# Kernel optimization log

Measured on AMD Instinct MI355X. Metric: run time of the kernel, lower is better.

Reference implementation:

```python
import math
import jax, jax.numpy as jnp
import numpy as np

B, S, HID = 1, 2048, 2048
NH, QLR, KVLR = 16, 1536, 512
QKD, QKP, VD = 128, 64, 128          # nope dim, rope dim, v dim
IH, ID, TOPK = 4, 128, 512            # indexer heads, indexer head dim, topk
EPS = 1e-6
NEG = -1e9
_MS = 0.1 * 1.0 * math.log(40.0) + 1.0           # mscale adjustment, rope_factor=40
SCALE = _MS * _MS / math.sqrt(QKD + QKP)          # main attention softmax scale
IDX_SCALE = ID ** -0.5                            # indexer softmax scale


def _freqs_cos_sin():
    # seqlen <= original_max_position_embeddings -> plain RoPE freqs (no YaRN branch)
    freqs = 1.0 / (10000.0 ** (jnp.arange(0, QKP, 2, dtype=jnp.float32) / QKP))  # [QKP/2]
    ang = jnp.outer(jnp.arange(S, dtype=jnp.float32), freqs)                      # [S, QKP/2]
    return jnp.cos(ang)[None, :, None, :], jnp.sin(ang)[None, :, None, :]         # [1,S,1,QKP/2]


def _rope_interleaved(x, cos, sin):
    # pairs are (x[..., 2i], x[..., 2i+1])
    x1, x2 = x[..., 0::2], x[..., 1::2]
    yr = x1 * cos - x2 * sin
    yi = x1 * sin + x2 * cos
    return jnp.stack([yr, yi], axis=-1).reshape(x.shape)


def _rope_half(x, cos, sin):
    # interleaved=False: real = first half, imag = second half; output [reals..., imags...]
    d2 = x.shape[-1] // 2
    x1, x2 = x[..., :d2], x[..., d2:]
    return jnp.concatenate([x1 * cos - x2 * sin, x1 * sin + x2 * cos], axis=-1)


def _rmsnorm(x, w):
    return x * jax.lax.rsqrt(jnp.mean(x * x, axis=-1, keepdims=True) + EPS) * w


def _layernorm(x, w, b):
    m = jnp.mean(x, axis=-1, keepdims=True)
    v = jnp.mean((x - m) ** 2, axis=-1, keepdims=True)
    return (x - m) * jax.lax.rsqrt(v + EPS) * w + b


def _indexer(x, qr, cos, sin, mask3, idx_wq_b, idx_wk, idx_kn_w, idx_kn_b, idx_ww):
    # x, qr detached by caller. mask3: [B,S,S]
    q = (qr @ idx_wq_b.T).reshape(B, S, IH, ID)
    q_pe, q_nope = q[..., :QKP], q[..., QKP:]
    q_pe = _rope_half(q_pe, cos, sin)
    q = jnp.concatenate([q_pe, q_nope], axis=-1)                   # [B,S,IH,ID]
    k = _layernorm(x @ idx_wk.T, idx_kn_w, idx_kn_b)               # [B,S,ID]
    k_pe, k_nope = k[..., :QKP], k[..., QKP:]
    k_pe = _rope_half(k_pe[:, :, None, :], cos, sin)[:, :, 0, :]
    k = jnp.concatenate([k_pe, k_nope], axis=-1)                   # [B,S,ID]
    weights = (x @ idx_ww.T) * (IH ** -0.5)                        # [B,S,IH]
    logits = jnp.einsum('bthd,bsd->bths', q, k) * IDX_SCALE        # [B,T,IH,S]
    logits = jax.nn.relu(logits)
    logits = jnp.einsum('bths,bth->bts', logits, weights)          # weighted head sum
    logits = logits + mask3
    topk_vals, topk_idx = jax.lax.top_k(logits, TOPK)
    log_topk_prob = jax.nn.log_softmax(topk_vals, axis=-1)
    return topk_idx, log_topk_prob


def reference(hidden_states, attention_mask, wq_down, q_ln_w, wq_up, wkv_down,
              kv_ln_w, wk_up, wv_up, wo, idx_wq_b, idx_wk, idx_kn_w, idx_kn_b, idx_ww):
    x = jnp.swapaxes(hidden_states, 0, 1)                          # [B,S,HID]
    mask3 = attention_mask[:, 0]                                   # [B,S,S]
    cos, sin = _freqs_cos_sin()

    qr = _rmsnorm(x @ wq_down.T, q_ln_w)                           # [B,S,QLR]
    q = (qr @ wq_up.T).reshape(B, S, NH, QKD + QKP)
    q_nope, q_pe = q[..., :QKD], q[..., QKD:]
    q_pe = _rope_interleaved(q_pe, cos, sin)

    kv = x @ wkv_down.T                                            # [B,S,KVLR+QKP]
    kv_c, k_pe = kv[..., :KVLR], kv[..., KVLR:]
    kv_c = _rmsnorm(kv_c, kv_ln_w)
    k_pe = _rope_interleaved(k_pe[:, :, None, :], cos, sin)        # [B,S,1,QKP]

    k_up_w = wk_up.reshape(NH, QKD, KVLR)
    q_abs = jnp.einsum('bshd,hdc->bshc', q_nope, k_up_w)           # absorbed q
    q_abs = jnp.concatenate([q_abs, q_pe], axis=-1)                # [B,S,NH,KVLR+QKP]

    topk_idx, log_topk_prob = _indexer(
        jax.lax.stop_gradient(x), jax.lax.stop_gradient(qr), cos, sin, mask3,
        idx_wq_b, idx_wk, idx_kn_w, idx_kn_b, idx_ww)

    keys = jnp.concatenate([kv_c, k_pe[:, :, 0, :]], axis=-1)      # [B,T,KVLR+QKP]
    scores = jnp.einsum('bshd,btd->bsht', q_abs, keys) * SCALE     # [B,S,NH,T]
    scores = scores + mask3[:, :, None, :]
    bi = jnp.arange(B)[:, None, None]
    si = jnp.arange(S)[None, :, None]
    index_mask = jnp.full((B, S, S), NEG, jnp.float32).at[bi, si, topk_idx].set(0.0)
    scores = scores + index_mask[:, :, None, :]
    probs = jax.nn.softmax(scores, axis=-1)                        # [B,S,NH,T]
    attn_out = jnp.einsum('bsht,btd->bshd', probs, kv_c)           # values = kv_c

    idx4 = jnp.broadcast_to(topk_idx[:, :, None, :], (B, S, NH, TOPK))
    sparse_probs = jnp.take_along_axis(jax.lax.stop_gradient(probs), idx4, axis=-1)
    attn_score = sparse_probs.sum(axis=2)
    attn_score = attn_score / attn_score.sum(axis=-1, keepdims=True)
    tgt = jnp.clip(jnp.log(attn_score), -100.0, 0.0)
    inp = jnp.clip(log_topk_prob, -100.0, 0.0)
    kl = jnp.sum(jnp.exp(tgt) * (tgt - inp))

    v_up_w = wv_up.reshape(NH, VD, KVLR)
    attn_out = jnp.einsum('bshc,hdc->bshd', attn_out, v_up_w)
    out = attn_out.reshape(B, S, NH * VD) @ wo.T
    return jnp.swapaxes(out, 0, 1), kl


def setup_inputs():
    key = jax.random.key(0)
    ks = jax.random.split(key, 12)
    p = lambda k, sh: jax.random.normal(k, sh, jnp.float32) * 0.02
    hidden_states = jax.random.normal(ks[0], (S, B, HID), jnp.float32)
    causal = jnp.where(jnp.arange(S)[:, None] >= jnp.arange(S)[None, :], 0.0, NEG).astype(jnp.float32)
    attention_mask = jnp.broadcast_to(causal, (B, 1, S, S))
    return dict(
        hidden_states=hidden_states,
        attention_mask=attention_mask,
        wq_down=p(ks[1], (QLR, HID)),
        q_ln_w=jnp.ones((QLR,), jnp.float32),
        wq_up=p(ks[2], (NH * (QKD + QKP), QLR)),
        wkv_down=p(ks[3], (KVLR + QKP, HID)),
        kv_ln_w=jnp.ones((KVLR,), jnp.float32),
        wk_up=p(ks[4], (NH * QKD, KVLR)),
        wv_up=p(ks[5], (NH * VD, KVLR)),
        wo=p(ks[6], (HID, NH * VD)),
        idx_wq_b=p(ks[7], (IH * ID, QLR)),
        idx_wk=p(ks[8], (ID, HID)),
        idx_kn_w=jnp.ones((ID,), jnp.float32),
        idx_kn_b=jnp.zeros((ID,), jnp.float32),
        idx_ww=p(ks[9], (IH, HID)),
    )
```

## Files before the change

kernel.cpp:

```cpp
#include <hip/hip_runtime.h>
#include <hip/hip_bf16.h>
#include <math.h>

typedef __hip_bfloat16 bf16;
typedef __attribute__((ext_vector_type(8))) short short8v;
typedef __attribute__((ext_vector_type(4))) float f32x4;

static constexpr float EPS_   = 1e-6f;
static constexpr float NEG_   = -1000000000.0f;
static constexpr float SCALE_ = 0.13523378f;
static constexpr float IDXSC_ = 0.08838834764832f;
static constexpr double LN10K_32 = 0.28782313662425575;

#define MFMA16(a, b, c) __builtin_amdgcn_mfma_f32_16x16x32_bf16(a, b, c, 0, 0, 0)

static __device__ float block_reduce_op(float v, int op) {
  __shared__ float red_s[16];
  int lane = threadIdx.x & 63, wid = threadIdx.x >> 6;
  #pragma unroll
  for (int off = 32; off > 0; off >>= 1) {
    float o = __shfl_down(v, off);
    v = op ? fmaxf(v, o) : (v + o);
  }
  __syncthreads();
  if (lane == 0) red_s[wid] = v;
  __syncthreads();
  if (threadIdx.x == 0) {
    int nw = ((int)blockDim.x + 63) >> 6;
    float r = red_s[0];
    for (int i = 1; i < nw; i++) r = op ? fmaxf(r, red_s[i]) : (r + red_s[i]);
    red_s[0] = r;
  }
  __syncthreads();
  return red_s[0];
}

__global__ __launch_bounds__(256) void f2b_kernel(const float* __restrict__ in,
                                                  bf16* __restrict__ out, long n) {
  long i = ((long)blockIdx.x * 256 + threadIdx.x) * 4;
  if (i + 3 < n) {
    float4 v = *(const float4*)(in + i);
    out[i] = __float2bfloat16(v.x); out[i+1] = __float2bfloat16(v.y);
    out[i+2] = __float2bfloat16(v.z); out[i+3] = __float2bfloat16(v.w);
  } else {
    for (int j = 0; j < 4 && i + j < n; j++) out[i+j] = __float2bfloat16(in[i+j]);
  }
}

template <int BT, int OB>
__global__ __launch_bounds__(256) void gemm_bf16(
    const bf16* __restrict__ A, const bf16* __restrict__ B, void* __restrict__ Cv,
    int M, int N, int K, int lda, int ldb, int ldc, long sA, long sB, long sC) {
  A += (long)blockIdx.z * sA;
  B += (long)blockIdx.z * sB;
  __shared__ bf16 As[128][40];
  __shared__ bf16 Bs[128][40];
  const int m0 = blockIdx.y * 128, n0 = blockIdx.x * 128;
  const int tid = threadIdx.x;
  const int wave = tid >> 6, lane = tid & 63, g = lane >> 4, li = lane & 15;
  const int mB = (wave >> 1) * 64, nB = (wave & 1) * 64;
  f32x4 acc[4][4];
  #pragma unroll
  for (int i = 0; i < 4; i++)
    #pragma unroll
    for (int j = 0; j < 4; j++) acc[i][j] = (f32x4){0.f, 0.f, 0.f, 0.f};

  for (int k0 = 0; k0 < K; k0 += 32) {
    {
      int row = tid >> 1, ko = (tid & 1) * 16;
      const bf16* src = A + (long)(m0 + row) * lda + k0 + ko;
      *(short8v*)&As[row][ko]     = *(const short8v*)src;
      *(short8v*)&As[row][ko + 8] = *(const short8v*)(src + 8);
    }
    if (BT) {
      int row = tid >> 1, ko = (tid & 1) * 16;
      int rr = n0 + row; if (rr >= N) rr = N - 1;
      const bf16* src = B + (long)rr * ldb + k0 + ko;
      *(short8v*)&Bs[row][ko]     = *(const short8v*)src;
      *(short8v*)&Bs[row][ko + 8] = *(const short8v*)(src + 8);
    } else {
      int k = tid >> 3, nb = (tid & 7) * 16;
      const bf16* src = B + (long)(k0 + k) * ldb + n0 + nb;
      short8v v0 = *(const short8v*)src;
      short8v v1 = *(const short8v*)(src + 8);
      #pragma unroll
      for (int j = 0; j < 8; j++) {
        Bs[nb + j][k]     = ((const bf16*)&v0)[j];
        Bs[nb + 8 + j][k] = ((const bf16*)&v1)[j];
      }
    }
    __syncthreads();
    short8v af[4], bfr[4];
    #pragma unroll
    for (int mt = 0; mt < 4; mt++) af[mt]  = *(const short8v*)&As[mB + mt*16 + li][g*8];
    #pragma unroll
    for (int nt = 0; nt < 4; nt++) bfr[nt] = *(const short8v*)&Bs[nB + nt*16 + li][g*8];
    #pragma unroll
    for (int mt = 0; mt < 4; mt++)
      #pragma unroll
      for (int nt = 0; nt < 4; nt++)
        acc[mt][nt] = MFMA16(af[mt], bfr[nt], acc[mt][nt]);
    __syncthreads();
  }
  #pragma unroll
  for (int mt = 0; mt < 4; mt++)
    #pragma unroll
    for (int nt = 0; nt < 4; nt++)
      #pragma unroll
      for (int r = 0; r < 4; r++) {
        int row = m0 + mB + mt*16 + g*4 + r;
        int col = n0 + nB + nt*16 + li;
        if (col < N) {
          long off = (long)blockIdx.z * sC + (long)row * ldc + col;
          if (OB) ((bf16*)Cv)[off] = __float2bfloat16(acc[mt][nt][r]);
          else    ((float*)Cv)[off] = acc[mt][nt][r];
        }
      }
}

__global__ __launch_bounds__(256) void rmsnorm_b_kernel(const float* __restrict__ x,
                                                        const float* __restrict__ w,
                                                        bf16* __restrict__ out, int D) {
  const float* r = x + (long)blockIdx.x * D;
  bf16* o = out + (long)blockIdx.x * D;
  float ss = 0.f;
  for (int i = threadIdx.x; i < D; i += 256) { float v = r[i]; ss = fmaf(v, v, ss); }
  ss = block_reduce_op(ss, 0);
  float sc = rsqrtf(ss / (float)D + EPS_);
  for (int i = threadIdx.x; i < D; i += 256) o[i] = __float2bfloat16(r[i] * sc * w[i]);
}

__global__ __launch_bounds__(256) void kv_norm_rope_kernel(const float* __restrict__ kv,
                                                           const float* __restrict__ w,
                                                           bf16* __restrict__ keys_b,
                                                           bf16* __restrict__ keysT_b) {
  int s = blockIdx.x;
  const float* r = kv + (long)s * 576;
  float ss = 0.f;
  for (int i = threadIdx.x; i < 512; i += 256) { float v = r[i]; ss = fmaf(v, v, ss); }
  ss = block_reduce_op(ss, 0);
  float sc = rsqrtf(ss / 512.f + EPS_);
  for (int i = threadIdx.x; i < 512; i += 256) {
    float v = r[i] * sc * w[i];
    bf16 b = __float2bfloat16(v);
    keys_b[(long)s * 576 + i] = b;
    keysT_b[(long)i * 2048 + s] = b;
  }
  if (threadIdx.x < 32) {
    int j = threadIdx.x;
    float f = (float)exp(-(double)j * LN10K_32);
    float ang = (float)s * f;
    float c = cosf(ang), sn = sinf(ang);
    float x1 = r[512 + 2*j], x2 = r[512 + 2*j + 1];
    keys_b[(long)s * 576 + 512 + 2*j]     = __float2bfloat16(x1 * c - x2 * sn);
    keys_b[(long)s * 576 + 512 + 2*j + 1] = __float2bfloat16(x1 * sn + x2 * c);
  }
}

__global__ __launch_bounds__(256) void rope_q_kernel(const bf16* __restrict__ q,
                                                     bf16* __restrict__ qabs) {
  int idx = blockIdx.x * 256 + threadIdx.x;
  int j = idx & 31, h = (idx >> 5) & 15, s = idx >> 9;
  float f = (float)exp(-(double)j * LN10K_32);
  float ang = (float)s * f;
  float c = cosf(ang), sn = sinf(ang);
  const bf16* src = q + (long)s * 3072 + h * 192 + 128;
  float x1 = __bfloat162float(src[2*j]), x2 = __bfloat162float(src[2*j+1]);
  bf16* dst = qabs + (long)s * 9216 + h * 576 + 512;
  dst[2*j]     = __float2bfloat16(x1 * c - x2 * sn);
  dst[2*j + 1] = __float2bfloat16(x1 * sn + x2 * c);
}

__global__ __launch_bounds__(256) void rope_qi_kernel(bf16* __restrict__ qi) {
  int idx = blockIdx.x * 256 + threadIdx.x;
  int j = idx & 31, ih = (idx >> 5) & 3, s = idx >> 7;
  float f = (float)exp(-(double)j * LN10K_32);
  float ang = (float)s * f;
  float c = cosf(ang), sn = sinf(ang);
  bf16* p = qi + (long)s * 512 + ih * 128;
  float x1 = __bfloat162float(p[j]), x2 = __bfloat162float(p[32 + j]);
  p[j]      = __float2bfloat16(x1 * c - x2 * sn);
  p[32 + j] = __float2bfloat16(x1 * sn + x2 * c);
}

__global__ __launch_bounds__(128) void ki_ln_rope_kernel(const float* __restrict__ kt,
                                                         const float* __restrict__ w,
                                                         const float* __restrict__ b,
                                                         bf16* __restrict__ ki_b) {
  int s = blockIdx.x, d = threadIdx.x;
  float v = kt[(long)s * 128 + d];
  float m = block_reduce_op(v, 0) * (1.f / 128.f);
  float dv = v - m;
  float var = block_reduce_op(dv * dv, 0) * (1.f / 128.f);
  float y = dv * rsqrtf(var + EPS_) * w[d] + b[d];
  __shared__ float ys[128];
  ys[d] = y;
  __syncthreads();
  float out;
  if (d < 64) {
    int j = d & 31;
    float f = (float)exp(-(double)j * LN10K_32);
    float ang = (float)s * f;
    float c = cosf(ang), sn = sinf(ang);
    float x1 = ys[j], x2 = ys[32 + j];
    out = (d < 32) ? (x1 * c - x2 * sn) : (x1 * sn + x2 * c);
  } else out = y;
  ki_b[(long)s * 128 + d] = __float2bfloat16(out);
}

__global__ __launch_bounds__(256) void wgt_kernel(const float* __restrict__ x,
                                                  const float* __restrict__ ww,
                                                  float* __restrict__ wgt) {
  int s = blockIdx.x;
  float a0 = 0, a1 = 0, a2 = 0, a3 = 0;
  for (int i = threadIdx.x; i < 2048; i += 256) {
    float xv = x[(long)s * 2048 + i];
    a0 = fmaf(xv, ww[i], a0);
    a1 = fmaf(xv, ww[2048 + i], a1);
    a2 = fmaf(xv, ww[4096 + i], a2);
    a3 = fmaf(xv, ww[6144 + i], a3);
  }
  a0 = block_reduce_op(a0, 0);
  a1 = block_reduce_op(a1, 0);
  a2 = block_reduce_op(a2, 0);
  a3 = block_reduce_op(a3, 0);
  if (threadIdx.x == 0) {
    wgt[s*4+0] = 0.5f*a0; wgt[s*4+1] = 0.5f*a1; wgt[s*4+2] = 0.5f*a2; wgt[s*4+3] = 0.5f*a3;
  }
}

__global__ __launch_bounds__(256) void idx_logits_mfma(const bf16* __restrict__ qi,
                                                       const bf16* __restrict__ ki,
                                                       const float* __restrict__ wgt,
                                                       float* __restrict__ logits) {
  const int t0 = blockIdx.y * 64, s0 = blockIdx.x * 128;
  const int tid = threadIdx.x, wave = tid >> 6, lane = tid & 63;
  const int g = lane >> 4, li = lane & 15;
  if (s0 > t0 + 63) {
    #pragma unroll
    for (int j = 0; j < 8; j++)
      #pragma unroll
      for (int r = 0; r < 4; r++) {
        int t = t0 + wave*16 + g*4 + r, sidx = s0 + j*16 + li;
        logits[(long)t * 2048 + sidx] = NEG_;
      }
    return;
  }
  f32x4 acc[8];
  #pragma unroll
  for (int j = 0; j < 8; j++) acc[j] = (f32x4){0.f,0.f,0.f,0.f};
  #pragma unroll
  for (int h = 0; h < 4; h++) {
    f32x4 tmp[8];
    #pragma unroll
    for (int j = 0; j < 8; j++) tmp[j] = (f32x4){0.f,0.f,0.f,0.f};
    const bf16* arow = qi + ((long)(t0 + wave*16 + li) * 4 + h) * 128 + g*8;
    #pragma unroll
    for (int ks = 0; ks < 4; ks++) {
      short8v a = *(const short8v*)(arow + ks*32);
      #pragma unroll
      for (int j = 0; j < 8; j++) {
        const bf16* brow = ki + (long)(s0 + j*16 + li) * 128 + ks*32 + g*8;
        tmp[j] = MFMA16(a, *(const short8v*)brow, tmp[j]);
      }
    }
    #pragma unroll
    for (int r = 0; r < 4; r++) {
      float wv = wgt[(t0 + wave*16 + g*4 + r)*4 + h];
      #pragma unroll
      for (int j = 0; j < 8; j++)
        acc[j][r] += fmaxf(tmp[j][r] * IDXSC_, 0.f) * wv;
    }
  }
  #pragma unroll
  for (int j = 0; j < 8; j++)
    #pragma unroll
    for (int r = 0; r < 4; r++) {
      int t = t0 + wave*16 + g*4 + r, sidx = s0 + j*16 + li;
      logits[(long)t * 2048 + sidx] = acc[j][r] + (sidx <= t ? 0.f : NEG_);
    }
}

__global__ __launch_bounds__(256) void topk_kernel(const float* __restrict__ logits,
                                                   int* __restrict__ tki,
                                                   float* __restrict__ tkv,
                                                   float* __restrict__ logZ) {
  int t = blockIdx.x;
  __shared__ unsigned skeys[2048];
  __shared__ unsigned hist[256];
  __shared__ float svals[512];
  __shared__ int s_want;
  __shared__ unsigned s_prefix;
  const float* row = logits + (long)t * 2048;
  for (int i = threadIdx.x; i < 2048; i += 256) {
    unsigned u = __float_as_uint(row[i]);
    skeys[i] = (u & 0x80000000u) ? ~u : (u | 0x80000000u);
  }
  if (threadIdx.x == 0) { s_want = 512; s_prefix = 0u; }
  __syncthreads();
  for (int shift = 24; shift >= 0; shift -= 8) {
    if (threadIdx.x < 256) hist[threadIdx.x] = 0u;
    __syncthreads();
    unsigned pmask = (shift == 24) ? 0u : (0xFFFFFFFFu << (shift + 8));
    unsigned pref = s_prefix;
    for (int i = threadIdx.x; i < 2048; i += 256) {
      unsigned k = skeys[i];
      if ((k & pmask) == pref) atomicAdd(&hist[(k >> shift) & 255u], 1u);
    }
    __syncthreads();
    if (threadIdx.x == 0) {
      int want = s_want;
      unsigned cum = 0;
      int b = 255;
      for (;; b--) {
        cum += hist[b];
        if ((int)cum >= want || b == 0) break;
      }
      s_want = want - (int)(cum - hist[b]);
      s_prefix = pref | ((unsigned)b << shift);
    }
    __syncthreads();
  }
  unsigned T = s_prefix;
  int want_eq = s_want;
  int c_gt = 512 - want_eq;
  if (threadIdx.x < 64) {
    int n_gt = 0, n_eq = 0;
    unsigned long long below = (1ull << threadIdx.x) - 1ull;
    for (int base = 0; base < 2048; base += 64) {
      int i = base + (int)threadIdx.x;
      unsigned k = skeys[i];
      bool gt = (k > T), eq = (k == T);
      unsigned long long bg = __ballot(gt);
      unsigned long long be = __ballot(eq);
      int slot = -1;
      if (gt) slot = n_gt + (int)__popcll(bg & below);
      else if (eq) {
        int er = n_eq + (int)__popcll(be & below);
        if (er < want_eq) slot = c_gt + er;
      }
      if (slot >= 0) {
        unsigned bits = (k & 0x80000000u) ? (k ^ 0x80000000u) : ~k;
        float val = __uint_as_float(bits);
        tki[(long)t * 512 + slot] = i;
        tkv[(long)t * 512 + slot] = val;
        svals[slot] = val;
      }
      n_gt += (int)__popcll(bg);
      n_eq += (int)__popcll(be);
    }
  }
  __syncthreads();
  float m = -3.4e38f;
  for (int i = threadIdx.x; i < 512; i += 256) m = fmaxf(m, svals[i]);
  m = block_reduce_op(m, 1);
  float se = 0.f;
  for (int i = threadIdx.x; i < 512; i += 256) se += expf(svals[i] - m);
  se = block_reduce_op(se, 0);
  if (threadIdx.x == 0) logZ[t] = m + logf(se);
}

__global__ __launch_bounds__(256, 4) void attn_mfma(
    const bf16* __restrict__ qabs, const bf16* __restrict__ keys,
    const bf16* __restrict__ keysT, const int* __restrict__ tki,
    const float* __restrict__ tkv, const float* __restrict__ logZ,
    bf16* __restrict__ aoc, float* __restrict__ kl) {
  const int s = blockIdx.x, tid = threadIdx.x;
  const int wave = tid >> 6, lane = tid & 63, g = lane >> 4, li = lane & 15;
  __shared__ int idxs[512];
  __shared__ __align__(16) bf16 qs[16 * 576];
  __shared__ __align__(16) bf16 ph[16 * 512];
  __shared__ float red[64];
  __shared__ float mxf[16], dnf[16];

  for (int i = tid; i < 512; i += 256) idxs[i] = tki[(long)s * 512 + i];
  for (int c = tid; c < 1152; c += 256) {
    int h = c / 72, off = (c % 72) * 8;
    const short8v v = *(const short8v*)(qabs + (long)s * 9216 + h * 576 + off);
    int byte = (h * 1152 + off * 2) ^ ((h & 7) << 4);
    *(short8v*)((char*)qs + byte) = v;
  }
  __syncthreads();

  f32x4 accS[8];
  int kid[8];
  const bf16* kr[8];
  #pragma unroll
  for (int j = 0; j < 8; j++) {
    accS[j] = (f32x4){0.f,0.f,0.f,0.f};
    kid[j] = idxs[(wave * 8 + j) * 16 + li];
    kr[j] = keys + (long)kid[j] * 576 + g * 8;
  }
  short8v kf[8];
  #pragma unroll
  for (int j = 0; j < 8; j++) kf[j] = *(const short8v*)kr[j];
  for (int ks = 0; ks < 18; ks++) {
    short8v a = *(const short8v*)((char*)qs + ((li * 1152 + (ks*32 + g*8) * 2) ^ ((li & 7) << 4)));
    short8v nx[8];
    const int nko = (ks < 17 ? ks + 1 : 17) * 32;
    #pragma unroll
    for (int j = 0; j < 8; j++) nx[j] = *(const short8v*)(kr[j] + nko);
    #pragma unroll
    for (int j = 0; j < 8; j++) accS[j] = MFMA16(a, kf[j], accS[j]);
    #pragma unroll
    for (int j = 0; j < 8; j++) kf[j] = nx[j];
  }

  float e[8][4];
  float m4[4];
  #pragma unroll
  for (int r = 0; r < 4; r++) m4[r] = -3.4e38f;
  #pragma unroll
  for (int j = 0; j < 8; j++) {
    float mask = (kid[j] <= s) ? 0.f : NEG_;
    #pragma unroll
    for (int r = 0; r < 4; r++) {
      e[j][r] = accS[j][r] * SCALE_ + mask;
      m4[r] = fmaxf(m4[r], e[j][r]);
    }
  }
  #pragma unroll
  for (int d = 1; d < 16; d <<= 1)
    #pragma unroll
    for (int r = 0; r < 4; r++) m4[r] = fmaxf(m4[r], __shfl_xor(m4[r], d));
  if (li == 0)
    #pragma unroll
    for (int r = 0; r < 4; r++) red[wave * 16 + g * 4 + r] = m4[r];
  __syncthreads();
  if (tid < 16) mxf[tid] = fmaxf(fmaxf(red[tid], red[16 + tid]), fmaxf(red[32 + tid], red[48 + tid]));
  __syncthreads();
  float d4[4] = {0.f, 0.f, 0.f, 0.f};
  #pragma unroll
  for (int j = 0; j < 8; j++)
    #pragma unroll
    for (int r = 0; r < 4; r++) {
      e[j][r] = __expf(e[j][r] - mxf[g * 4 + r]);
      d4[r] += e[j][r];
    }
  #pragma unroll
  for (int d = 1; d < 16; d <<= 1)
    #pragma unroll
    for (int r = 0; r < 4; r++) d4[r] += __shfl_xor(d4[r], d);
  if (li == 0)
    #pragma unroll
    for (int r = 0; r < 4; r++) red[wave * 16 + g * 4 + r] = d4[r];
  __syncthreads();
  if (tid < 16) dnf[tid] = red[tid] + red[16 + tid] + red[32 + tid] + red[48 + tid];
  __syncthreads();

  float invd[4];
  #pragma unroll
  for (int r = 0; r < 4; r++) invd[r] = 1.f / dnf[g * 4 + r];
  float tasj[8];
  #pragma unroll
  for (int j = 0; j < 8; j++) {
    float t = 0.f;
    #pragma unroll
    for (int r = 0; r < 4; r++) t += e[j][r] * invd[r];
    t += __shfl_xor(t, 16);
    t += __shfl_xor(t, 32);
    tasj[j] = t;
  }
  float klacc = 0.f;
  if (g == 0) {
    float lz = logZ[s];
    #pragma unroll
    for (int j = 0; j < 8; j++) {
      int slot = (wave * 8 + j) * 16 + li;
      float tgt = fminf(fmaxf(logf(tasj[j] * 0.0625f), -100.f), 0.f);
      float inp = fminf(fmaxf(tkv[(long)s * 512 + slot] - lz, -100.f), 0.f);
      klacc += expf(tgt) * (tgt - inp);
    }
  }
  #pragma unroll
  for (int d = 1; d < 16; d <<= 1) klacc += __shfl_xor(klacc, d);
  if (lane == 0) atomicAdd(kl, klacc);

  f32x4 accO[8];
  #pragma unroll
  for (int j = 0; j < 8; j++) accO[j] = (f32x4){0.f,0.f,0.f,0.f};
  for (int c = 0; c < 4; c++) {
    const int base = c << 9;
    if (base > s) break;
    __syncthreads();
    { uint4 z = {0,0,0,0};
      for (int i = tid; i < 1024; i += 256) ((uint4*)ph)[i] = z; }
    __syncthreads();
    #pragma unroll
    for (int j = 0; j < 8; j++) {
      int kk = kid[j] - base;
      if (0 <= kk && kk < 512) {
        #pragma unroll
        for (int r = 0; r < 4; r++) {
          int h = g * 4 + r;
          int byte = (h * 1024 + kk * 2) ^ ((h & 7) << 4);
          *(bf16*)((char*)ph + byte) = __float2bfloat16(e[j][r]);
        }
      }
    }
    __syncthreads();
    const int KT = (min(512, s - base + 1) + 31) >> 5;
    for (int kt = 0; kt < KT; kt++) {
      short8v a = *(const short8v*)((char*)ph + ((li * 1024 + (kt*32 + g*8) * 2) ^ ((li & 7) << 4)));
      #pragma unroll
      for (int j = 0; j < 8; j++) {
        const bf16* bp = keysT + (long)(wave * 128 + j * 16 + li) * 2048 + base + kt*32 + g*8;
        accO[j] = MFMA16(a, *(const short8v*)bp, accO[j]);
      }
    }
  }
  __syncthreads();
  #pragma unroll
  for (int j = 0; j < 8; j++)
    #pragma unroll
    for (int r = 0; r < 4; r++) {
      int h = g * 4 + r, dim = wave * 128 + j * 16 + li;
      aoc[(long)s * 8192 + h * 512 + dim] = __float2bfloat16(accO[j][r] / dnf[h]);
    }
}

__global__ void zero_kernel(float* p) {
  if (threadIdx.x == 0 && blockIdx.x == 0) p[0] = 0.f;
}
__global__ void copykl_kernel(const float* src, float* dst) { dst[0] = src[0]; }

extern "C" void kernel_launch(void* const* d_in, const int* in_sizes, int n_in,
                              void* d_out, int out_size, void* d_ws, size_t ws_size,
                              hipStream_t stream) {
  (void)in_sizes; (void)n_in; (void)out_size; (void)ws_size;
  const float* x        = (const float*)d_in[0];
  const float* wq_down  = (const float*)d_in[2];
  const float* q_ln_w   = (const float*)d_in[3];
  const float* wq_up    = (const float*)d_in[4];
  const float* wkv_down = (const float*)d_in[5];
  const float* kv_ln_w  = (const float*)d_in[6];
  const float* wk_up    = (const float*)d_in[7];
  const float* wv_up    = (const float*)d_in[8];
  const float* wo       = (const float*)d_in[9];
  const float* idx_wq_b = (const float*)d_in[10];
  const float* idx_wk   = (const float*)d_in[11];
  const float* idx_kn_w = (const float*)d_in[12];
  const float* idx_kn_b = (const float*)d_in[13];
  const float* idx_ww   = (const float*)d_in[14];
  float* out = (float*)d_out;

  char* w = (char*)d_ws;
  size_t off = 0;
  auto alloc = [&](size_t bytes) { void* p = w + off; off += (bytes + 255) & ~255ul; return p; };
  float* qr     = (float*)alloc(2048L*1536*4);
  float* kvtmp  = (float*)alloc(2048L*576*4);
  float* kitmp  = (float*)alloc(2048L*128*4);
  float* logits = (float*)alloc(2048L*2048*4);
  float* tkv    = (float*)alloc(2048L*512*4);
  float* logZ   = (float*)alloc(2048*4);
  float* wgt    = (float*)alloc(2048L*4*4);
  float* klbuf  = (float*)alloc(64);
  int*   tki    = (int*)alloc(2048L*512*4);
  bf16* x_b     = (bf16*)alloc(2048L*2048*2);
  bf16* qr_b    = (bf16*)alloc(2048L*1536*2);
  bf16* q_b     = (bf16*)alloc(2048L*3072*2);
  bf16* qabs_b  = (bf16*)alloc(2048L*9216*2);
  bf16* keys_b  = (bf16*)alloc(2048L*576*2);
  bf16* keysT_b = (bf16*)alloc(512L*2048*2);
  bf16* qi_b    = (bf16*)alloc(2048L*512*2);
  bf16* ki_b    = (bf16*)alloc(2048L*128*2);
  bf16* aoc_b   = (bf16*)alloc(2048L*8192*2);
  bf16* ao_b    = (bf16*)alloc(2048L*2048*2);
  bf16* wqd_b   = (bf16*)alloc(1536L*2048*2);
  bf16* wqu_b   = (bf16*)alloc(3072L*1536*2);
  bf16* wkv_b   = (bf16*)alloc(576L*2048*2);
  bf16* wku_b   = (bf16*)alloc(16L*128*512*2);
  bf16* wvu_b   = (bf16*)alloc(16L*128*512*2);
  bf16* wo_b    = (bf16*)alloc(2048L*2048*2);
  bf16* iwq_b   = (bf16*)alloc(512L*1536*2);
  bf16* iwk_b   = (bf16*)alloc(128L*2048*2);

  dim3 b256(256);
  auto cvt = [&](const float* src, bf16* dst, long n) {
    f2b_kernel<<<(int)((n + 1023) / 1024), b256, 0, stream>>>(src, dst, n);
  };
  cvt(x, x_b, 2048L*2048);
  cvt(wq_down, wqd_b, 1536L*2048);
  cvt(wq_up, wqu_b, 3072L*1536);
  cvt(wkv_down, wkv_b, 576L*2048);
  cvt(wk_up, wku_b, 16L*128*512);
  cvt(wv_up, wvu_b, 16L*128*512);
  cvt(wo, wo_b, 2048L*2048);
  cvt(idx_wq_b, iwq_b, 512L*1536);
  cvt(idx_wk, iwk_b, 128L*2048);

  gemm_bf16<1,0><<<dim3(12,16), b256, 0, stream>>>(x_b, wqd_b, qr, 2048,1536,2048, 2048,2048,1536, 0,0,0);
  rmsnorm_b_kernel<<<2048, b256, 0, stream>>>(qr, q_ln_w, qr_b, 1536);
  gemm_bf16<1,1><<<dim3(24,16), b256, 0, stream>>>(qr_b, wqu_b, q_b, 2048,3072,1536, 1536,1536,3072, 0,0,0);
  gemm_bf16<1,0><<<dim3(5,16), b256, 0, stream>>>(x_b, wkv_b, kvtmp, 2048,576,2048, 2048,2048,576, 0,0,0);
  kv_norm_rope_kernel<<<2048, b256, 0, stream>>>(kvtmp, kv_ln_w, keys_b, keysT_b);
  rope_q_kernel<<<4096, b256, 0, stream>>>(q_b, qabs_b);
  gemm_bf16<0,1><<<dim3(4,16,16), b256, 0, stream>>>(q_b, wku_b, qabs_b, 2048,512,128, 3072,512,9216, 192, 128L*512, 576);
  gemm_bf16<1,1><<<dim3(4,16), b256, 0, stream>>>(qr_b, iwq_b, qi_b, 2048,512,1536, 1536,1536,512, 0,0,0);
  rope_qi_kernel<<<1024, b256, 0, stream>>>(qi_b);
  gemm_bf16<1,0><<<dim3(1,16), b256, 0, stream>>>(x_b, iwk_b, kitmp, 2048,128,2048, 2048,2048,128, 0,0,0);
  ki_ln_rope_kernel<<<2048, dim3(128), 0, stream>>>(kitmp, idx_kn_w, idx_kn_b, ki_b);
  wgt_kernel<<<2048, b256, 0, stream>>>(x, idx_ww, wgt);
  idx_logits_mfma<<<dim3(16,32), b256, 0, stream>>>(qi_b, ki_b, wgt, logits);
  topk_kernel<<<2048, b256, 0, stream>>>(logits, tki, tkv, logZ);
  zero_kernel<<<1, 64, 0, stream>>>(klbuf);
  attn_mfma<<<2048, b256, 0, stream>>>(qabs_b, keys_b, keysT_b, tki, tkv, logZ, aoc_b, klbuf);
  gemm_bf16<1,1><<<dim3(1,16,16), b256, 0, stream>>>(aoc_b, wvu_b, ao_b, 2048,128,512, 8192,512,2048, 512, 128L*512, 128);
  gemm_bf16<1,0><<<dim3(16,16), b256, 0, stream>>>(ao_b, wo_b, out, 2048,2048,2048, 2048,2048,2048, 0,0,0);
  copykl_kernel<<<1, 1, 0, stream>>>(klbuf, out + 4194304L);
}
```

Baseline: 1.051 ms.

## Split sparse attention into score kernel and blocked causal P·V GEMM

The fused attention kernel is split in two. The first computes scores and softmax, then writes normalized sparse probabilities into dense per-128-row causal blocks of a global P buffer. The second does P·V as a tiled MFMA GEMM per head and row block, reading keys directly so the transposed key copy is no longer built. Query fragments are also read straight from global memory instead of staged in LDS, and blocks run in reverse order so heavy rows start first. The cost is a large extra write and read of the P buffer, with scratch reused over dead workspace, in exchange for better reuse of V across the 128 rows in each block.

```diff
diff --git a/kernel.cpp b/kernel.cpp
--- a/kernel.cpp
+++ b/kernel.cpp
@@ -132,20 +132,15 @@
 
 __global__ __launch_bounds__(256) void kv_norm_rope_kernel(const float* __restrict__ kv,
                                                            const float* __restrict__ w,
-                                                           bf16* __restrict__ keys_b,
-                                                           bf16* __restrict__ keysT_b) {
+                                                           bf16* __restrict__ keys_b) {
   int s = blockIdx.x;
   const float* r = kv + (long)s * 576;
   float ss = 0.f;
   for (int i = threadIdx.x; i < 512; i += 256) { float v = r[i]; ss = fmaf(v, v, ss); }
   ss = block_reduce_op(ss, 0);
   float sc = rsqrtf(ss / 512.f + EPS_);
-  for (int i = threadIdx.x; i < 512; i += 256) {
-    float v = r[i] * sc * w[i];
-    bf16 b = __float2bfloat16(v);
-    keys_b[(long)s * 576 + i] = b;
-    keysT_b[(long)i * 2048 + s] = b;
-  }
+  for (int i = threadIdx.x; i < 512; i += 256)
+    keys_b[(long)s * 576 + i] = __float2bfloat16(r[i] * sc * w[i]);
   if (threadIdx.x < 32) {
     int j = threadIdx.x;
     float f = (float)exp(-(double)j * LN10K_32);
@@ -360,28 +355,23 @@
   if (threadIdx.x == 0) logZ[t] = m + logf(se);
 }
 
-__global__ __launch_bounds__(256, 4) void attn_mfma(
+__global__ __launch_bounds__(256, 4) void attn_qk(
     const bf16* __restrict__ qabs, const bf16* __restrict__ keys,
-    const bf16* __restrict__ keysT, const int* __restrict__ tki,
-    const float* __restrict__ tkv, const float* __restrict__ logZ,
-    bf16* __restrict__ aoc, float* __restrict__ kl) {
-  const int s = blockIdx.x, tid = threadIdx.x;
+    const int* __restrict__ tki, const float* __restrict__ tkv,
+    const float* __restrict__ logZ, bf16* __restrict__ Pg,
+    float* __restrict__ kl) {
+  const int s = 2047 - blockIdx.x;
+  const int tid = threadIdx.x;
   const int wave = tid >> 6, lane = tid & 63, g = lane >> 4, li = lane & 15;
   __shared__ int idxs[512];
-  __shared__ __align__(16) bf16 qs[16 * 576];
   __shared__ __align__(16) bf16 ph[16 * 512];
   __shared__ float red[64];
   __shared__ float mxf[16], dnf[16];
 
   for (int i = tid; i < 512; i += 256) idxs[i] = tki[(long)s * 512 + i];
-  for (int c = tid; c < 1152; c += 256) {
-    int h = c / 72, off = (c % 72) * 8;
-    const short8v v = *(const short8v*)(qabs + (long)s * 9216 + h * 576 + off);
-    int byte = (h * 1152 + off * 2) ^ ((h & 7) << 4);
-    *(short8v*)((char*)qs + byte) = v;
-  }
-  __syncthreads();
-
+  __syncthreads();
+
+  const bf16* qrow = qabs + (long)s * 9216 + li * 576 + g * 8;
   f32x4 accS[8];
   int kid[8];
   const bf16* kr[8];
@@ -391,17 +381,19 @@
     kid[j] = idxs[(wave * 8 + j) * 16 + li];
     kr[j] = keys + (long)kid[j] * 576 + g * 8;
   }
+  short8v af = *(const short8v*)qrow;
   short8v kf[8];
   #pragma unroll
   for (int j = 0; j < 8; j++) kf[j] = *(const short8v*)kr[j];
   for (int ks = 0; ks < 18; ks++) {
-    short8v a = *(const short8v*)((char*)qs + ((li * 1152 + (ks*32 + g*8) * 2) ^ ((li & 7) << 4)));
+    const int nko = (ks < 17 ? ks + 1 : 17) * 32;
+    short8v afn = *(const short8v*)(qrow + nko);
     short8v nx[8];
-    const int nko = (ks < 17 ? ks + 1 : 17) * 32;
     #pragma unroll
     for (int j = 0; j < 8; j++) nx[j] = *(const short8v*)(kr[j] + nko);
     #pragma unroll
-    for (int j = 0; j < 8; j++) accS[j] = MFMA16(a, kf[j], accS[j]);
+    for (int j = 0; j < 8; j++) accS[j] = MFMA16(af, kf[j], accS[j]);
+    af = afn;
     #pragma unroll
     for (int j = 0; j < 8; j++) kf[j] = nx[j];
   }
@@ -451,6 +443,7 @@
   float invd[4];
   #pragma unroll
   for (int r = 0; r < 4; r++) invd[r] = 1.f / dnf[g * 4 + r];
+
   float tasj[8];
   #pragma unroll
   for (int j = 0; j < 8; j++) {
@@ -476,12 +469,12 @@
   for (int d = 1; d < 16; d <<= 1) klacc += __shfl_xor(klacc, d);
   if (lane == 0) atomicAdd(kl, klacc);
 
-  f32x4 accO[8];
-  #pragma unroll
-  for (int j = 0; j < 8; j++) accO[j] = (f32x4){0.f,0.f,0.f,0.f};
-  for (int c = 0; c < 4; c++) {
-    const int base = c << 9;
-    if (base > s) break;
+  const int m = s >> 7;
+  const int Km = (m + 1) << 7;
+  const int rr = s & 127;
+  bf16* Pbase = Pg + 131072L * m * (m + 1);
+  for (int base = 0; base < Km; base += 512) {
+    const int cw = min(512, Km - base);
     __syncthreads();
     { uint4 z = {0,0,0,0};
       for (int i = tid; i < 1024; i += 256) ((uint4*)ph)[i] = z; }
@@ -491,32 +484,80 @@
       int kk = kid[j] - base;
       if (0 <= kk && kk < 512) {
         #pragma unroll
-        for (int r = 0; r < 4; r++) {
-          int h = g * 4 + r;
-          int byte = (h * 1024 + kk * 2) ^ ((h & 7) << 4);
-          *(bf16*)((char*)ph + byte) = __float2bfloat16(e[j][r]);
-        }
-      }
-    }
-    __syncthreads();
-    const int KT = (min(512, s - base + 1) + 31) >> 5;
-    for (int kt = 0; kt < KT; kt++) {
-      short8v a = *(const short8v*)((char*)ph + ((li * 1024 + (kt*32 + g*8) * 2) ^ ((li & 7) << 4)));
+        for (int r = 0; r < 4; r++)
+          ph[(g * 4 + r) * 512 + kk] = __float2bfloat16(e[j][r] * invd[r]);
+      }
+    }
+    __syncthreads();
+    for (int u = tid; u < 1024; u += 256) {
+      int h = u >> 6, c = (u & 63) * 8;
+      if (c < cw)
+        *(short8v*)(Pbase + ((long)(h * 128 + rr) * Km + base + c)) =
+            *(const short8v*)&ph[h * 512 + c];
+    }
+  }
+}
+
+__global__ __launch_bounds__(256) void attn_pv(const bf16* __restrict__ Pg,
+                                               const bf16* __restrict__ keys,
+                                               bf16* __restrict__ aoc) {
+  const int m = 15 - blockIdx.y;
+  const int h = blockIdx.z;
+  const int Km = (m + 1) << 7;
+  const bf16* A = Pg + 131072L * m * (m + 1) + (long)h * 128 * Km;
+  const int n0 = blockIdx.x * 128;
+  __shared__ bf16 As[128][40];
+  __shared__ bf16 Bs[128][40];
+  const int tid = threadIdx.x;
+  const int wave = tid >> 6, lane = tid & 63, g = lane >> 4, li = lane & 15;
+  const int mB = (wave >> 1) * 64, nB = (wave & 1) * 64;
+  f32x4 acc[4][4];
+  #pragma unroll
+  for (int i = 0; i < 4; i++)
+    #pragma unroll
+    for (int j = 0; j < 4; j++) acc[i][j] = (f32x4){0.f, 0.f, 0.f, 0.f};
+
+  for (int k0 = 0; k0 < Km; k0 += 32) {
+    {
+      int row = tid >> 1, ko = (tid & 1) * 16;
+      const bf16* src = A + (long)row * Km + k0 + ko;
+      *(short8v*)&As[row][ko]     = *(const short8v*)src;
+      *(short8v*)&As[row][ko + 8] = *(const short8v*)(src + 8);
+    }
+    {
+      int k = tid >> 3, nb = (tid & 7) * 16;
+      const bf16* src = keys + (long)(k0 + k) * 576 + n0 + nb;
+      short8v v0 = *(const short8v*)src;
+      short8v v1 = *(const short8v*)(src + 8);
       #pragma unroll
       for (int j = 0; j < 8; j++) {
-        const bf16* bp = keysT + (long)(wave * 128 + j * 16 + li) * 2048 + base + kt*32 + g*8;
-        accO[j] = MFMA16(a, *(const short8v*)bp, accO[j]);
-      }
-    }
-  }
-  __syncthreads();
-  #pragma unroll
-  for (int j = 0; j < 8; j++)
-    #pragma unroll
-    for (int r = 0; r < 4; r++) {
-      int h = g * 4 + r, dim = wave * 128 + j * 16 + li;
-      aoc[(long)s * 8192 + h * 512 + dim] = __float2bfloat16(accO[j][r] / dnf[h]);
-    }
+        Bs[nb + j][k]     = ((const bf16*)&v0)[j];
+        Bs[nb + 8 + j][k] = ((const bf16*)&v1)[j];
+      }
+    }
+    __syncthreads();
+    short8v af[4], bfr[4];
+    #pragma unroll
+    for (int mt = 0; mt < 4; mt++) af[mt]  = *(const short8v*)&As[mB + mt*16 + li][g*8];
+    #pragma unroll
+    for (int nt = 0; nt < 4; nt++) bfr[nt] = *(const short8v*)&Bs[nB + nt*16 + li][g*8];
+    #pragma unroll
+    for (int mt = 0; mt < 4; mt++)
+      #pragma unroll
+      for (int nt = 0; nt < 4; nt++)
+        acc[mt][nt] = MFMA16(af[mt], bfr[nt], acc[mt][nt]);
+    __syncthreads();
+  }
+  #pragma unroll
+  for (int mt = 0; mt < 4; mt++)
+    #pragma unroll
+    for (int nt = 0; nt < 4; nt++)
+      #pragma unroll
+      for (int r = 0; r < 4; r++) {
+        int row = m * 128 + mB + mt*16 + g*4 + r;
+        int col = n0 + nB + nt*16 + li;
+        aoc[(long)row * 8192 + h * 512 + col] = __float2bfloat16(acc[mt][nt][r]);
+      }
 }
 
 __global__ void zero_kernel(float* p) {
@@ -547,33 +588,36 @@
   char* w = (char*)d_ws;
   size_t off = 0;
   auto alloc = [&](size_t bytes) { void* p = w + off; off += (bytes + 255) & ~255ul; return p; };
+  bf16* keys_b  = (bf16*)alloc(2048L*576*2);
+  bf16* qabs_b  = (bf16*)alloc(2048L*9216*2);
+  bf16* aoc_b   = (bf16*)alloc(2048L*8192*2);
+  bf16* ao_b    = (bf16*)alloc(2048L*2048*2);
+  bf16* wvu_b   = (bf16*)alloc(16L*128*512*2);
+  bf16* wo_b    = (bf16*)alloc(2048L*2048*2);
+  float* tkv    = (float*)alloc(2048L*512*4);
+  float* logZ   = (float*)alloc(2048*4);
+  float* klbuf  = (float*)alloc(64);
+  int*   tki    = (int*)alloc(2048L*512*4);
+  size_t scratch0 = off;
+  bf16* Pg = (bf16*)(w + scratch0);
   float* qr     = (float*)alloc(2048L*1536*4);
   float* kvtmp  = (float*)alloc(2048L*576*4);
   float* kitmp  = (float*)alloc(2048L*128*4);
   float* logits = (float*)alloc(2048L*2048*4);
-  float* tkv    = (float*)alloc(2048L*512*4);
-  float* logZ   = (float*)alloc(2048*4);
   float* wgt    = (float*)alloc(2048L*4*4);
-  float* klbuf  = (float*)alloc(64);
-  int*   tki    = (int*)alloc(2048L*512*4);
   bf16* x_b     = (bf16*)alloc(2048L*2048*2);
   bf16* qr_b    = (bf16*)alloc(2048L*1536*2);
   bf16* q_b     = (bf16*)alloc(2048L*3072*2);
-  bf16* qabs_b  = (bf16*)alloc(2048L*9216*2);
-  bf16* keys_b  = (bf16*)alloc(2048L*576*2);
-  bf16* keysT_b = (bf16*)alloc(512L*2048*2);
   bf16* qi_b    = (bf16*)alloc(2048L*512*2);
   bf16* ki_b    = (bf16*)alloc(2048L*128*2);
-  bf16* aoc_b   = (bf16*)alloc(2048L*8192*2);
-  bf16* ao_b    = (bf16*)alloc(2048L*2048*2);
   bf16* wqd_b   = (bf16*)alloc(1536L*2048*2);
   bf16* wqu_b   = (bf16*)alloc(3072L*1536*2);
   bf16* wkv_b   = (bf16*)alloc(576L*2048*2);
   bf16* wku_b   = (bf16*)alloc(16L*128*512*2);
-  bf16* wvu_b   = (bf16*)alloc(16L*128*512*2);
-  bf16* wo_b    = (bf16*)alloc(2048L*2048*2);
   bf16* iwq_b   = (bf16*)alloc(512L*1536*2);
   bf16* iwk_b   = (bf16*)alloc(128L*2048*2);
+  size_t pg_end = scratch0 + 131072ul*16*17*2;
+  if (off < pg_end) off = pg_end;
 
   dim3 b256(256);
   auto cvt = [&](const float* src, bf16* dst, long n) {
@@ -593,7 +637,7 @@
   rmsnorm_b_kernel<<<2048, b256, 0, stream>>>(qr, q_ln_w, qr_b, 1536);
   gemm_bf16<1,1><<<dim3(24,16), b256, 0, stream>>>(qr_b, wqu_b, q_b, 2048,3072,1536, 1536,1536,3072, 0,0,0);
   gemm_bf16<1,0><<<dim3(5,16), b256, 0, stream>>>(x_b, wkv_b, kvtmp, 2048,576,2048, 2048,2048,576, 0,0,0);
-  kv_norm_rope_kernel<<<2048, b256, 0, stream>>>(kvtmp, kv_ln_w, keys_b, keysT_b);
+  kv_norm_rope_kernel<<<2048, b256, 0, stream>>>(kvtmp, kv_ln_w, keys_b);
   rope_q_kernel<<<4096, b256, 0, stream>>>(q_b, qabs_b);
   gemm_bf16<0,1><<<dim3(4,16,16), b256, 0, stream>>>(q_b, wku_b, qabs_b, 2048,512,128, 3072,512,9216, 192, 128L*512, 576);
   gemm_bf16<1,1><<<dim3(4,16), b256, 0, stream>>>(qr_b, iwq_b, qi_b, 2048,512,1536, 1536,1536,512, 0,0,0);
@@ -604,7 +648,8 @@
   idx_logits_mfma<<<dim3(16,32), b256, 0, stream>>>(qi_b, ki_b, wgt, logits);
   topk_kernel<<<2048, b256, 0, stream>>>(logits, tki, tkv, logZ);
   zero_kernel<<<1, 64, 0, stream>>>(klbuf);
-  attn_mfma<<<2048, b256, 0, stream>>>(qabs_b, keys_b, keysT_b, tki, tkv, logZ, aoc_b, klbuf);
+  attn_qk<<<2048, b256, 0, stream>>>(qabs_b, keys_b, tki, tkv, logZ, Pg, klbuf);
+  attn_pv<<<dim3(4,16,16), b256, 0, stream>>>(Pg, keys_b, aoc_b);
   gemm_bf16<1,1><<<dim3(1,16,16), b256, 0, stream>>>(aoc_b, wvu_b, ao_b, 2048,128,512, 8192,512,2048, 512, 128L*512, 128);
   gemm_bf16<1,0><<<dim3(16,16), b256, 0, stream>>>(ao_b, wo_b, out, 2048,2048,2048, 2048,2048,2048, 0,0,0);
   copykl_kernel<<<1, 1, 0, stream>>>(klbuf, out + 4194304L);
```

Result: faster. 970.3 us (-7.7%).
